# Performance work log

Hardware: AMD Instinct MI355X
Metric: run time of the kernel (lower is better)

## Reference

```python
import jax, jax.numpy as jnp
import numpy as np

H, W = 512, 512
CHUNK = 128            # gaussians blended per scan step
BLUR = 0.3             # antialiasing dilation (as in 3DGS EWA low-pass)
ALPHA_MIN = 1.0 / 255.0
ALPHA_MAX = 0.99


def setup_inputs() -> dict:
    key = jax.random.key(0)
    k = jax.random.split(key, 6)
    N = 8192
    means2D = jax.random.uniform(k[0], (N, 2), jnp.float32) * jnp.array([W, H], jnp.float32)
    colors = jax.random.uniform(k[1], (N, 3), jnp.float32)
    opacities = jax.random.uniform(k[2], (N, 1), jnp.float32)
    scales = jax.random.uniform(k[3], (N, 2), jnp.float32) * 15.0 + 1.0   # pixels
    rotations = jax.random.uniform(k[4], (N, 1), jnp.float32) * (2.0 * np.pi)
    depths = jax.random.uniform(k[5], (N,), jnp.float32)
    background = jnp.zeros((3,), jnp.float32)
    return dict(means2D=means2D, colors=colors, opacities=opacities,
                scales=scales, rotations=rotations, depths=depths,
                background=background)


def _rasterize(means2D, colors, opacities, scales, rotations, depths, background):
    # depth sort: front (small depth) first
    order = jnp.argsort(depths)
    m = means2D[order]                 # [N,2] (x,y)
    col = colors[order]                # [N,3]
    op = opacities[order][:, 0]        # [N]
    s = scales[order]                  # [N,2]
    th = rotations[order][:, 0]        # [N]

    # 2D covariance  Sigma = R diag(s^2) R^T
    c, si = jnp.cos(th), jnp.sin(th)
    sx2, sy2 = s[:, 0] ** 2, s[:, 1] ** 2
    A = c * c * sx2 + si * si * sy2
    Cc = si * si * sx2 + c * c * sy2
    B = c * si * (sx2 - sy2)
    det = A * Cc - B * B
    # antialiasing: dilate covariance, compensate opacity
    A2, C2 = A + BLUR, Cc + BLUR
    det2 = A2 * C2 - B * B
    op = op * jnp.sqrt(jnp.maximum(det / det2, 0.0))
    invdet = 1.0 / det2
    ia, ib, ic = C2 * invdet, -B * invdet, A2 * invdet   # Sigma^-1 entries

    # pixel centers
    ys, xs = jnp.meshgrid(jnp.arange(H, dtype=jnp.float32) + 0.5,
                          jnp.arange(W, dtype=jnp.float32) + 0.5, indexing='ij')

    N = m.shape[0]
    nchunk = N // CHUNK
    chunk = lambda a: a.reshape((nchunk, CHUNK) + a.shape[1:])
    gs = (chunk(m), chunk(col), chunk(op), chunk(ia), chunk(ib), chunk(ic))

    def step(carry, g):
        T, acc = carry                       # T:[H,W] transmittance, acc:[3,H,W]
        gm, gcol, gop, gia, gib, gic = g     # per-chunk [C,...]
        dx = xs[None] - gm[:, 0, None, None]                 # [C,H,W]
        dy = ys[None] - gm[:, 1, None, None]
        power = (-0.5 * (gia[:, None, None] * dx * dx + gic[:, None, None] * dy * dy)
                 - gib[:, None, None] * dx * dy)
        alpha = jnp.minimum(ALPHA_MAX, gop[:, None, None] * jnp.exp(power))
        alpha = jnp.where(alpha < ALPHA_MIN, 0.0, alpha)     # skip tiny splats (as CUDA)
        one_m = 1.0 - alpha
        cum = jnp.cumprod(one_m, axis=0)                     # inclusive
        Twithin = jnp.concatenate([jnp.ones_like(cum[:1]), cum[:-1]], 0)  # exclusive
        w = alpha * Twithin * T[None]                        # blend weight per gaussian
        acc = acc + jnp.einsum('nc,nhw->chw', gcol, w)
        T = T * cum[-1]
        return (T, acc), None

    init = (jnp.ones((H, W), jnp.float32), jnp.zeros((3, H, W), jnp.float32))
    (T, acc), _ = jax.lax.scan(step, init, gs)
    color = acc + background[:, None, None] * T[None]        # [3,H,W]
    return color


def reference(means2D, colors, opacities, scales, rotations, depths, background):
    return _rasterize(means2D, colors, opacities, scales, rotations, depths, background)
```

## Files before the change

kernel.cpp:

```cpp
#include <hip/hip_runtime.h>
#include <hip/hip_fp16.h>
#include <stdint.h>

#define HH 512
#define WW 512
#define ALPHA_MIN_C (1.0f/255.0f)
#define ALPHA_MAX_C 0.99f
#define BLUR_C 0.3f
#define TERM_EPS 1.0e-4f
#define LOG2E 1.4426950408889634f

#define JSL 512
__global__ __launch_bounds__(256) void rank_kernel(const float* __restrict__ depths,
                                                   int N, int* __restrict__ partial) {
    __shared__ uint32_t sk[JSL];
    const int tid = threadIdx.x;
    const int ngb = N >> 8;
    const int gb = blockIdx.x % ngb;
    const int jb = blockIdx.x / ngb;
    const int j0 = jb * JSL;
    for (int i = tid; i < JSL; i += 256)
        sk[i] = __float_as_uint(depths[j0 + i]);
    __syncthreads();
    const int g = gb * 256 + tid;
    const uint32_t mb = __float_as_uint(depths[g]);
    const int glim = g - j0;
    int cnt = 0;
    const uint4* sk4 = (const uint4*)sk;
#pragma unroll 8
    for (int q = 0; q < JSL / 4; ++q) {
        uint4 v = sk4[q];
        const int i4 = q * 4;
        cnt += (v.x < mb) || (v.x == mb && (i4 + 0) < glim);
        cnt += (v.y < mb) || (v.y == mb && (i4 + 1) < glim);
        cnt += (v.z < mb) || (v.z == mb && (i4 + 2) < glim);
        cnt += (v.w < mb) || (v.w == mb && (i4 + 3) < glim);
    }
    partial[jb * N + g] = cnt;
}

__global__ __launch_bounds__(256) void prep_kernel(
    const float* __restrict__ means, const float* __restrict__ colors,
    const float* __restrict__ ops, const float* __restrict__ scales,
    const float* __restrict__ rots, const int* __restrict__ partial, int N,
    float4* __restrict__ pP, float4* __restrict__ pQ) {
    int g = blockIdx.x * 256 + threadIdx.x;
    if (g >= N) return;
    int pos = 0;
#pragma unroll
    for (int s = 0; s < 16; ++s) pos += partial[s * N + g];
    float mx = means[2*g], my = means[2*g+1];
    float th = rots[g];
    float c = cosf(th), si = sinf(th);
    float sx = scales[2*g], sy = scales[2*g+1];
    float sx2 = sx*sx, sy2 = sy*sy;
    float A  = c*c*sx2 + si*si*sy2;
    float Cc = si*si*sx2 + c*c*sy2;
    float B  = c*si*(sx2 - sy2);
    float det = A*Cc - B*B;
    float A2 = A + BLUR_C, C2 = Cc + BLUR_C;
    float det2 = A2*C2 - B*B;
    float op = ops[g] * sqrtf(fmaxf(det/det2, 0.0f));
    float invd = 1.0f/det2;
    float ia = C2*invd, ib = -B*invd, ic = A2*invd;
    float iaF = -0.5f*LOG2E*ia, icF = -0.5f*LOG2E*ic, ibF = -LOG2E*ib;
    float mid = 0.5f*(A2+C2);
    float lam = mid + sqrtf(fmaxf(mid*mid - det2, 0.0f));
    float r2;
    if (op < ALPHA_MIN_C) {
        r2 = -1.0f;
    } else {
        float t = __logf(op * 255.0f);
        r2 = fmaxf(2.0f * lam * t, 0.0f) * 1.0001f + 0.25f;
    }
    __half2 h2 = __floats2half2_rn(ibF, icF);
    unsigned ibic; __builtin_memcpy(&ibic, &h2, 4);
    unsigned r10 = __float2uint_rn(fminf(colors[3*g  ], 1.0f) * 1023.0f);
    unsigned g10 = __float2uint_rn(fminf(colors[3*g+1], 1.0f) * 1023.0f);
    unsigned b10 = __float2uint_rn(fminf(colors[3*g+2], 1.0f) * 1023.0f);
    unsigned rgb = r10 | (g10 << 10) | (b10 << 20);
    pP[pos] = make_float4(mx, my, r2, op);
    pQ[pos] = make_float4(iaF, __uint_as_float(ibic), __uint_as_float(rgb), 0.0f);
}

__global__ __launch_bounds__(128) void blend_kernel(
    const float4* __restrict__ pP, const float4* __restrict__ pQ,
    const float* __restrict__ bg, int N, float* __restrict__ out) {
    __shared__ __align__(16) float sG[2][2*128*8];
    __shared__ __align__(8)  int swcnt[2][2];
    const int tid = threadIdx.x;
    const int lane = tid & 63, w = tid >> 6;
    const int tileX = blockIdx.x & 31, tileY = blockIdx.x >> 5;
    const int px = tileX*16 + (tid & 15);
    const int py = tileY*16 + (tid >> 4);
    const float fx = px + 0.5f, fy = py + 0.5f;
    const float x0 = tileX*16 + 0.5f, x1 = x0 + 15.0f;
    const float y0 = tileY*16 + 0.5f, y1 = y0 + 15.0f;
    const uint64_t lmlt = (1ull << lane) - 1ull;
    float T0 = 1.0f, T1 = 1.0f;
    float aR0=0.f,aG0=0.f,aB0=0.f,aR1=0.f,aG1=0.f,aB1=0.f;
    const int nch = N >> 8;
    const int gofs = (w << 7) + lane;

    float4 a0 = pP[gofs],    q0 = pQ[gofs];
    float4 a1 = pP[gofs+64], q1 = pQ[gofs+64];
    {
        float nx = fminf(fmaxf(a0.x,x0),x1)-a0.x, ny = fminf(fmaxf(a0.y,y0),y1)-a0.y;
        bool f0 = (nx*nx + ny*ny) <= a0.z;
        nx = fminf(fmaxf(a1.x,x0),x1)-a1.x; ny = fminf(fmaxf(a1.y,y0),y1)-a1.y;
        bool f1 = (nx*nx + ny*ny) <= a1.z;
        uint64_t m0 = __ballot(f0);
        if (f0) { float* rec = &sG[0][(w*128 + __popcll(m0 & lmlt))*8];
                  *(float4*)rec = make_float4(a0.x,a0.y,q0.x,q0.y);
                  *(float2*)(rec+4) = make_float2(a0.w,q0.z); }
        int c0 = (int)__popcll(m0);
        uint64_t m1 = __ballot(f1);
        if (f1) { float* rec = &sG[0][(w*128 + c0 + __popcll(m1 & lmlt))*8];
                  *(float4*)rec = make_float4(a1.x,a1.y,q1.x,q1.y);
                  *(float2*)(rec+4) = make_float2(a1.w,q1.z); }
        if (lane == 0) swcnt[0][w] = c0 + (int)__popcll(m1);
    }
    {   const int g = 256 + gofs;
        if (g < N) { a0 = pP[g]; q0 = pQ[g]; a1 = pP[g+64]; q1 = pQ[g+64]; } }
    __syncthreads();

    int cur = 0;
    for (int k = 0; k < nch; ++k) {
        const int nxt = cur ^ 1;
        if (k + 1 < nch) {
            float nx = fminf(fmaxf(a0.x,x0),x1)-a0.x, ny = fminf(fmaxf(a0.y,y0),y1)-a0.y;
            bool f0 = (nx*nx + ny*ny) <= a0.z;
            nx = fminf(fmaxf(a1.x,x0),x1)-a1.x; ny = fminf(fmaxf(a1.y,y0),y1)-a1.y;
            bool f1 = (nx*nx + ny*ny) <= a1.z;
            uint64_t m0 = __ballot(f0);
            if (f0) { float* rec = &sG[nxt][(w*128 + __popcll(m0 & lmlt))*8];
                      *(float4*)rec = make_float4(a0.x,a0.y,q0.x,q0.y);
                      *(float2*)(rec+4) = make_float2(a0.w,q0.z); }
            int c0 = (int)__popcll(m0);
            uint64_t m1 = __ballot(f1);
            if (f1) { float* rec = &sG[nxt][(w*128 + c0 + __popcll(m1 & lmlt))*8];
                      *(float4*)rec = make_float4(a1.x,a1.y,q1.x,q1.y);
                      *(float2*)(rec+4) = make_float2(a1.w,q1.z); }
            if (lane == 0) swcnt[nxt][w] = c0 + (int)__popcll(m1);
            const int g = (k + 2) * 256 + gofs;
            if (g < N) { a0 = pP[g]; q0 = pQ[g]; a1 = pP[g+64]; q1 = pQ[g+64]; }
        }
        if (!__all((T0 < TERM_EPS) & (T1 < TERM_EPS))) {
            const int cA = swcnt[cur][0], cB = swcnt[cur][1];
#pragma unroll
            for (int s = 0; s < 2; ++s) {
                const int cnt = (s == 0) ? cA : cB;
                const float* seg = &sG[cur][s*128*8];
                for (int i = 0; i < cnt; ++i) {
                    const float4 r0 = *(const float4*)(seg + i*8);
                    const float2 r1 = *(const float2*)(seg + i*8 + 4);
                    float dx  = fx - r0.x;
                    float dy  = fy - r0.y;
                    float dyB = dy + 8.0f;
                    unsigned hh = __float_as_uint(r0.w);
                    __half2 h2; __builtin_memcpy(&h2, &hh, 4);
                    float ibv = __half2float(h2.x);
                    float icv = __half2float(h2.y);
                    float bse = r0.z * (dx*dx);
                    float pb  = ibv * dx;
                    float p0 = fmaf(icv, dy*dy,   fmaf(pb, dy,  bse));
                    float p1 = fmaf(icv, dyB*dyB, fmaf(pb, dyB, bse));
                    float al0 = fminf(ALPHA_MAX_C, r1.x * exp2f(p0));
                    float al1 = fminf(ALPHA_MAX_C, r1.x * exp2f(p1));
                    al0 = (al0 >= ALPHA_MIN_C) ? al0 : 0.0f;
                    al1 = (al1 >= ALPHA_MIN_C) ? al1 : 0.0f;
                    if (__any((al0 > 0.0f) | (al1 > 0.0f))) {
                        unsigned rgb = __float_as_uint(r1.y);
                        float cr = (float)(rgb & 1023u);
                        float cg = (float)((rgb >> 10) & 1023u);
                        float cb = (float)((rgb >> 20) & 1023u);
                        float s0 = al0 * T0 * (1.0f/1023.0f);
                        float s1 = al1 * T1 * (1.0f/1023.0f);
                        aR0 = fmaf(cr, s0, aR0); aG0 = fmaf(cg, s0, aG0); aB0 = fmaf(cb, s0, aB0);
                        aR1 = fmaf(cr, s1, aR1); aG1 = fmaf(cg, s1, aG1); aB1 = fmaf(cb, s1, aB1);
                        T0 = fmaf(-al0, T0, T0);
                        T1 = fmaf(-al1, T1, T1);
                    }
                }
            }
        }
        if (__syncthreads_and((T0 < TERM_EPS) & (T1 < TERM_EPS))) break;
        cur = nxt;
    }
    const float b0 = bg[0], b1 = bg[1], b2 = bg[2];
    const int pix0 = py*WW + px;
    const int pix1 = pix0 + 8*WW;
    out[pix0]            = aR0 + b0*T0;
    out[pix0 +   HH*WW]  = aG0 + b1*T0;
    out[pix0 + 2*HH*WW]  = aB0 + b2*T0;
    out[pix1]            = aR1 + b0*T1;
    out[pix1 +   HH*WW]  = aG1 + b1*T1;
    out[pix1 + 2*HH*WW]  = aB1 + b2*T1;
}

extern "C" void kernel_launch(void* const* d_in, const int* in_sizes, int n_in,
                              void* d_out, int out_size, void* d_ws, size_t ws_size,
                              hipStream_t stream) {
    const float* means   = (const float*)d_in[0];
    const float* colors  = (const float*)d_in[1];
    const float* ops     = (const float*)d_in[2];
    const float* scales  = (const float*)d_in[3];
    const float* rots    = (const float*)d_in[4];
    const float* depths  = (const float*)d_in[5];
    const float* bg      = (const float*)d_in[6];
    const int N = in_sizes[0] / 2;

    char* ws = (char*)d_ws;
    float4* pP    = (float4*)(ws);
    float4* pQ    = (float4*)(ws + (size_t)N*16);
    int*    part  = (int*)  (ws + (size_t)N*32);

    const int ngb = N / 256;
    const int njb = N / JSL;
    rank_kernel<<<dim3(ngb*njb), dim3(256), 0, stream>>>(depths, N, part);
    prep_kernel<<<dim3((N+255)/256), dim3(256), 0, stream>>>(
        means, colors, ops, scales, rots, part, N, pP, pQ);
    blend_kernel<<<dim3((WW/16)*(HH/16)), dim3(128), 0, stream>>>(
        pP, pQ, bg, N, (float*)d_out);
}
```

Measured before the change: 154.9 us.

## Split gaussian list into depth segments blended in parallel, then composite

Replaces the single per-tile blend with a two-stage scheme. Four depth-ordered segments of 2048 gaussians are blended independently per tile by 64-thread blocks, each thread handling four pixels. Partial colour and transmittance are stored as fp16 and merged front-to-back by a new composite kernel. This adds parallelism across the gaussian axis and drops block-level syncs, but it loses early termination across segments, adds a workspace round trip and an extra launch, and reduces precision through fp16 intermediates.

Measured after the change: 134.3 us. 1.15x faster.

```diff
diff --git a/kernel.cpp b/kernel.cpp
--- a/kernel.cpp
+++ b/kernel.cpp
@@ -4,6 +4,7 @@
 
 #define HH 512
 #define WW 512
+#define NPIX (HH*WW)
 #define ALPHA_MIN_C (1.0f/255.0f)
 #define ALPHA_MAX_C 0.99f
 #define BLUR_C 0.3f
@@ -83,119 +84,158 @@
     pQ[pos] = make_float4(iaF, __uint_as_float(ibic), __uint_as_float(rgb), 0.0f);
 }
 
-__global__ __launch_bounds__(128) void blend_kernel(
+#define NSEG 4
+#define SEGG 2048
+#define CHK  128
+#define NCHK (SEGG/CHK)
+
+__device__ __forceinline__ uint2 packAT(float r, float g, float b, float t) {
+    __half2 hrg = __floats2half2_rn(r, g);
+    __half2 hbt = __floats2half2_rn(b, t);
+    uint2 u;
+    __builtin_memcpy(&u.x, &hrg, 4);
+    __builtin_memcpy(&u.y, &hbt, 4);
+    return u;
+}
+
+__global__ __launch_bounds__(64) void seg_blend_kernel(
     const float4* __restrict__ pP, const float4* __restrict__ pQ,
-    const float* __restrict__ bg, int N, float* __restrict__ out) {
-    __shared__ __align__(16) float sG[2][2*128*8];
-    __shared__ __align__(8)  int swcnt[2][2];
-    const int tid = threadIdx.x;
-    const int lane = tid & 63, w = tid >> 6;
-    const int tileX = blockIdx.x & 31, tileY = blockIdx.x >> 5;
-    const int px = tileX*16 + (tid & 15);
-    const int py = tileY*16 + (tid >> 4);
+    uint2* __restrict__ segbuf) {
+    __shared__ __align__(16) float sG[2][CHK*8];
+    const int lane = threadIdx.x;
+    const int tile = blockIdx.x & 1023;
+    const int seg  = blockIdx.x >> 10;
+    const int tX = tile & 31, tY = tile >> 5;
+    const int px = tX*16 + (lane & 15);
+    const int py = tY*16 + (lane >> 4);
     const float fx = px + 0.5f, fy = py + 0.5f;
-    const float x0 = tileX*16 + 0.5f, x1 = x0 + 15.0f;
-    const float y0 = tileY*16 + 0.5f, y1 = y0 + 15.0f;
-    const uint64_t lmlt = (1ull << lane) - 1ull;
-    float T0 = 1.0f, T1 = 1.0f;
-    float aR0=0.f,aG0=0.f,aB0=0.f,aR1=0.f,aG1=0.f,aB1=0.f;
-    const int nch = N >> 8;
-    const int gofs = (w << 7) + lane;
-
-    float4 a0 = pP[gofs],    q0 = pQ[gofs];
-    float4 a1 = pP[gofs+64], q1 = pQ[gofs+64];
+    const float x0 = tX*16 + 0.5f, x1 = x0 + 15.0f;
+    const float y0 = tY*16 + 0.5f, y1 = y0 + 15.0f;
+    const uint64_t lm = (1ull << lane) - 1ull;
+    float T0=1.f,T1=1.f,T2=1.f,T3=1.f;
+    float aR0=0.f,aG0=0.f,aB0=0.f;
+    float aR1=0.f,aG1=0.f,aB1=0.f;
+    float aR2=0.f,aG2=0.f,aB2=0.f;
+    float aR3=0.f,aG3=0.f,aB3=0.f;
+    const int gb = seg * SEGG;
+
+    float4 a0 = pP[gb+lane],    q0 = pQ[gb+lane];
+    float4 a1 = pP[gb+64+lane], q1 = pQ[gb+64+lane];
+    int cntA = 0, cntB = 0;
     {
         float nx = fminf(fmaxf(a0.x,x0),x1)-a0.x, ny = fminf(fmaxf(a0.y,y0),y1)-a0.y;
         bool f0 = (nx*nx + ny*ny) <= a0.z;
         nx = fminf(fmaxf(a1.x,x0),x1)-a1.x; ny = fminf(fmaxf(a1.y,y0),y1)-a1.y;
         bool f1 = (nx*nx + ny*ny) <= a1.z;
         uint64_t m0 = __ballot(f0);
-        if (f0) { float* rec = &sG[0][(w*128 + __popcll(m0 & lmlt))*8];
+        if (f0) { float* rec = &sG[0][__popcll(m0 & lm)*8];
                   *(float4*)rec = make_float4(a0.x,a0.y,q0.x,q0.y);
                   *(float2*)(rec+4) = make_float2(a0.w,q0.z); }
         int c0 = (int)__popcll(m0);
         uint64_t m1 = __ballot(f1);
-        if (f1) { float* rec = &sG[0][(w*128 + c0 + __popcll(m1 & lmlt))*8];
+        if (f1) { float* rec = &sG[0][(c0 + __popcll(m1 & lm))*8];
                   *(float4*)rec = make_float4(a1.x,a1.y,q1.x,q1.y);
                   *(float2*)(rec+4) = make_float2(a1.w,q1.z); }
-        if (lane == 0) swcnt[0][w] = c0 + (int)__popcll(m1);
-    }
-    {   const int g = 256 + gofs;
-        if (g < N) { a0 = pP[g]; q0 = pQ[g]; a1 = pP[g+64]; q1 = pQ[g+64]; } }
-    __syncthreads();
+        cntA = c0 + (int)__popcll(m1);
+    }
+    {   const int g = gb + CHK + lane;
+        a0 = pP[g]; q0 = pQ[g]; a1 = pP[g+64]; q1 = pQ[g+64]; }
 
     int cur = 0;
-    for (int k = 0; k < nch; ++k) {
+    for (int k = 0; k < NCHK; ++k) {
         const int nxt = cur ^ 1;
-        if (k + 1 < nch) {
+        if (k + 1 < NCHK) {
             float nx = fminf(fmaxf(a0.x,x0),x1)-a0.x, ny = fminf(fmaxf(a0.y,y0),y1)-a0.y;
             bool f0 = (nx*nx + ny*ny) <= a0.z;
             nx = fminf(fmaxf(a1.x,x0),x1)-a1.x; ny = fminf(fmaxf(a1.y,y0),y1)-a1.y;
             bool f1 = (nx*nx + ny*ny) <= a1.z;
             uint64_t m0 = __ballot(f0);
-            if (f0) { float* rec = &sG[nxt][(w*128 + __popcll(m0 & lmlt))*8];
+            if (f0) { float* rec = &sG[nxt][__popcll(m0 & lm)*8];
                       *(float4*)rec = make_float4(a0.x,a0.y,q0.x,q0.y);
                       *(float2*)(rec+4) = make_float2(a0.w,q0.z); }
             int c0 = (int)__popcll(m0);
             uint64_t m1 = __ballot(f1);
-            if (f1) { float* rec = &sG[nxt][(w*128 + c0 + __popcll(m1 & lmlt))*8];
+            if (f1) { float* rec = &sG[nxt][(c0 + __popcll(m1 & lm))*8];
                       *(float4*)rec = make_float4(a1.x,a1.y,q1.x,q1.y);
                       *(float2*)(rec+4) = make_float2(a1.w,q1.z); }
-            if (lane == 0) swcnt[nxt][w] = c0 + (int)__popcll(m1);
-            const int g = (k + 2) * 256 + gofs;
-            if (g < N) { a0 = pP[g]; q0 = pQ[g]; a1 = pP[g+64]; q1 = pQ[g+64]; }
-        }
-        if (!__all((T0 < TERM_EPS) & (T1 < TERM_EPS))) {
-            const int cA = swcnt[cur][0], cB = swcnt[cur][1];
-#pragma unroll
-            for (int s = 0; s < 2; ++s) {
-                const int cnt = (s == 0) ? cA : cB;
-                const float* seg = &sG[cur][s*128*8];
-                for (int i = 0; i < cnt; ++i) {
-                    const float4 r0 = *(const float4*)(seg + i*8);
-                    const float2 r1 = *(const float2*)(seg + i*8 + 4);
-                    float dx  = fx - r0.x;
-                    float dy  = fy - r0.y;
-                    float dyB = dy + 8.0f;
-                    unsigned hh = __float_as_uint(r0.w);
-                    __half2 h2; __builtin_memcpy(&h2, &hh, 4);
-                    float ibv = __half2float(h2.x);
-                    float icv = __half2float(h2.y);
-                    float bse = r0.z * (dx*dx);
-                    float pb  = ibv * dx;
-                    float p0 = fmaf(icv, dy*dy,   fmaf(pb, dy,  bse));
-                    float p1 = fmaf(icv, dyB*dyB, fmaf(pb, dyB, bse));
-                    float al0 = fminf(ALPHA_MAX_C, r1.x * exp2f(p0));
-                    float al1 = fminf(ALPHA_MAX_C, r1.x * exp2f(p1));
-                    al0 = (al0 >= ALPHA_MIN_C) ? al0 : 0.0f;
-                    al1 = (al1 >= ALPHA_MIN_C) ? al1 : 0.0f;
-                    if (__any((al0 > 0.0f) | (al1 > 0.0f))) {
-                        unsigned rgb = __float_as_uint(r1.y);
-                        float cr = (float)(rgb & 1023u);
-                        float cg = (float)((rgb >> 10) & 1023u);
-                        float cb = (float)((rgb >> 20) & 1023u);
-                        float s0 = al0 * T0 * (1.0f/1023.0f);
-                        float s1 = al1 * T1 * (1.0f/1023.0f);
-                        aR0 = fmaf(cr, s0, aR0); aG0 = fmaf(cg, s0, aG0); aB0 = fmaf(cb, s0, aB0);
-                        aR1 = fmaf(cr, s1, aR1); aG1 = fmaf(cg, s1, aG1); aB1 = fmaf(cb, s1, aB1);
-                        T0 = fmaf(-al0, T0, T0);
-                        T1 = fmaf(-al1, T1, T1);
-                    }
-                }
+            const int cn = c0 + (int)__popcll(m1);
+            if (nxt == 0) cntA = cn; else cntB = cn;
+            if (k + 2 < NCHK) {
+                const int g = gb + (k+2)*CHK + lane;
+                a0 = pP[g]; q0 = pQ[g]; a1 = pP[g+64]; q1 = pQ[g+64];
             }
         }
-        if (__syncthreads_and((T0 < TERM_EPS) & (T1 < TERM_EPS))) break;
+        const int cnt = (cur == 0) ? cntA : cntB;
+        const float* segp = sG[cur];
+        for (int i = 0; i < cnt; ++i) {
+            const float4 r0 = *(const float4*)(segp + i*8);
+            const float2 r1 = *(const float2*)(segp + i*8 + 4);
+            float dx = fx - r0.x;
+            float dy = fy - r0.y;
+            unsigned hh = __float_as_uint(r0.w);
+            __half2 h2; __builtin_memcpy(&h2, &hh, 4);
+            float ibv = __half2float(h2.x);
+            float icv = __half2float(h2.y);
+            float bse = r0.z * (dx*dx);
+            float pb  = ibv * dx;
+            float d1 = dy + 4.0f, d2 = dy + 8.0f, d3 = dy + 12.0f;
+            float p0 = fmaf(icv, dy*dy, fmaf(pb, dy, bse));
+            float p1 = fmaf(icv, d1*d1, fmaf(pb, d1, bse));
+            float p2 = fmaf(icv, d2*d2, fmaf(pb, d2, bse));
+            float p3 = fmaf(icv, d3*d3, fmaf(pb, d3, bse));
+            float al0 = fminf(ALPHA_MAX_C, r1.x * exp2f(p0));
+            float al1 = fminf(ALPHA_MAX_C, r1.x * exp2f(p1));
+            float al2 = fminf(ALPHA_MAX_C, r1.x * exp2f(p2));
+            float al3 = fminf(ALPHA_MAX_C, r1.x * exp2f(p3));
+            al0 = (al0 >= ALPHA_MIN_C) ? al0 : 0.0f;
+            al1 = (al1 >= ALPHA_MIN_C) ? al1 : 0.0f;
+            al2 = (al2 >= ALPHA_MIN_C) ? al2 : 0.0f;
+            al3 = (al3 >= ALPHA_MIN_C) ? al3 : 0.0f;
+            if (__any((al0 > 0.f) | (al1 > 0.f) | (al2 > 0.f) | (al3 > 0.f))) {
+                unsigned rgb = __float_as_uint(r1.y);
+                float cr = (float)(rgb & 1023u)         * (1.0f/1023.0f);
+                float cg = (float)((rgb >> 10) & 1023u) * (1.0f/1023.0f);
+                float cb = (float)((rgb >> 20) & 1023u) * (1.0f/1023.0f);
+                float s0 = al0*T0, s1 = al1*T1, s2 = al2*T2, s3 = al3*T3;
+                aR0 = fmaf(cr,s0,aR0); aG0 = fmaf(cg,s0,aG0); aB0 = fmaf(cb,s0,aB0);
+                aR1 = fmaf(cr,s1,aR1); aG1 = fmaf(cg,s1,aG1); aB1 = fmaf(cb,s1,aB1);
+                aR2 = fmaf(cr,s2,aR2); aG2 = fmaf(cg,s2,aG2); aB2 = fmaf(cb,s2,aB2);
+                aR3 = fmaf(cr,s3,aR3); aG3 = fmaf(cg,s3,aG3); aB3 = fmaf(cb,s3,aB3);
+                T0 = fmaf(-al0,T0,T0); T1 = fmaf(-al1,T1,T1);
+                T2 = fmaf(-al2,T2,T2); T3 = fmaf(-al3,T3,T3);
+            }
+        }
+        if (__all((T0 < TERM_EPS) & (T1 < TERM_EPS) &
+                  (T2 < TERM_EPS) & (T3 < TERM_EPS))) break;
         cur = nxt;
     }
-    const float b0 = bg[0], b1 = bg[1], b2 = bg[2];
     const int pix0 = py*WW + px;
-    const int pix1 = pix0 + 8*WW;
-    out[pix0]            = aR0 + b0*T0;
-    out[pix0 +   HH*WW]  = aG0 + b1*T0;
-    out[pix0 + 2*HH*WW]  = aB0 + b2*T0;
-    out[pix1]            = aR1 + b0*T1;
-    out[pix1 +   HH*WW]  = aG1 + b1*T1;
-    out[pix1 + 2*HH*WW]  = aB1 + b2*T1;
+    uint2* sb = segbuf + seg * NPIX;
+    sb[pix0        ] = packAT(aR0, aG0, aB0, T0);
+    sb[pix0 +  4*WW] = packAT(aR1, aG1, aB1, T1);
+    sb[pix0 +  8*WW] = packAT(aR2, aG2, aB2, T2);
+    sb[pix0 + 12*WW] = packAT(aR3, aG3, aB3, T3);
+}
+
+__global__ __launch_bounds__(256) void composite_kernel(
+    const uint2* __restrict__ segbuf, const float* __restrict__ bg,
+    float* __restrict__ out) {
+    const int pix = blockIdx.x * 256 + threadIdx.x;
+    float R = 0.f, G = 0.f, B = 0.f, T = 1.f;
+#pragma unroll
+    for (int s = 0; s < NSEG; ++s) {
+        uint2 v = segbuf[s * NPIX + pix];
+        __half2 hrg, hbt;
+        __builtin_memcpy(&hrg, &v.x, 4);
+        __builtin_memcpy(&hbt, &v.y, 4);
+        R = fmaf(T, __half2float(hrg.x), R);
+        G = fmaf(T, __half2float(hrg.y), G);
+        B = fmaf(T, __half2float(hbt.x), B);
+        T *= __half2float(hbt.y);
+    }
+    out[pix]          = R + bg[0]*T;
+    out[pix +   NPIX] = G + bg[1]*T;
+    out[pix + 2*NPIX] = B + bg[2]*T;
 }
 
 extern "C" void kernel_launch(void* const* d_in, const int* in_sizes, int n_in,
@@ -214,12 +254,14 @@
     float4* pP    = (float4*)(ws);
     float4* pQ    = (float4*)(ws + (size_t)N*16);
     int*    part  = (int*)  (ws + (size_t)N*32);
+    uint2*  segb  = (uint2*)(ws + (size_t)N*32 + (size_t)16*N*4);
 
     const int ngb = N / 256;
     const int njb = N / JSL;
     rank_kernel<<<dim3(ngb*njb), dim3(256), 0, stream>>>(depths, N, part);
     prep_kernel<<<dim3((N+255)/256), dim3(256), 0, stream>>>(
         means, colors, ops, scales, rots, part, N, pP, pQ);
-    blend_kernel<<<dim3((WW/16)*(HH/16)), dim3(128), 0, stream>>>(
-        pP, pQ, bg, N, (float*)d_out);
-}
+    seg_blend_kernel<<<dim3(NSEG*1024), dim3(64), 0, stream>>>(pP, pQ, segb);
+    composite_kernel<<<dim3(NPIX/256), dim3(256), 0, stream>>>(
+        segb, bg, (float*)d_out);
+}
```
